# Kernel optimization log

Hardware: AMD Instinct MI355X
Metric: run time of the kernel (lower is better)

## Reference

```python
import jax, jax.numpy as jnp
from jax import lax
import numpy as np

B, NG, NC = 4, 513, 512  # batch, grid size N, coef size N-1

_STENCILS = [[[-1/6, 2/3], [-1/3, -1/6]],
             [[2/3, -1/6], [-1/6, -1/3]],
             [[-1/6, -1/3], [2/3, -1/6]],
             [[-1/3, -1/6], [-1/6, 2/3]]]

def _kernel():
    # torch: vstack 4 (1,1,2,2) kernels -> permute(1,0,2,3) => (out=1, in=4, 2, 2)
    return jnp.asarray(_STENCILS, jnp.float32)[None]

def darcy(x, a, kernel):
    # x: (B,1,N,N), a: (B,1,N-1,N-1)
    N = x.shape[-1]
    X = jnp.concatenate([x[:, :, 1:N, :N-1] * a,
                         x[:, :, 1:N, 1:] * a,
                         x[:, :, :N-1, 1:] * a,
                         x[:, :, :N-1, :N-1] * a], axis=1)  # (B,4,N-1,N-1)
    Ax = lax.conv_general_dilated(X, kernel, (1, 1), 'VALID')  # (B,1,N-2,N-2)
    return jnp.pad(Ax, ((0, 0), (0, 0), (1, 1), (1, 1)))

def _conv3(x, w):
    # x: (Cin,H,W), w: (Cout,Cin,3,3), padding=1
    return lax.conv_general_dilated(x[None], w, (1, 1), ((1, 1), (1, 1)))[0]
_CONVB = jax.vmap(_conv3)

def mcc(x, w):
    # per-sample complex 3x3 conv == torch multi_channel_conv diagonal trick
    yr = _CONVB(x.real, w.real) - _CONVB(x.imag, w.imag)
    yi = _CONVB(x.real, w.imag) + _CONVB(x.imag, w.real)
    return yr + 1j * yi

def conjT(w):
    # transpose(-4,-3).transpose(-2,-1).conj()
    return jnp.conj(jnp.swapaxes(jnp.swapaxes(w, 1, 2), -2, -1))

def expand(r):
    Bb, C, M, N = r.shape
    Z = jnp.zeros((Bb, C, 2 * (M + 1), 2 * (N + 1)), r.dtype)
    Z = Z.at[:, :, 1:M+1, 1:N+1].set(r)
    Z = Z.at[:, :, M+2:, 1:N+1].set(-r[:, :, ::-1, :])
    Z = Z.at[:, :, 1:M+1, N+2:].set(-r[:, :, :, ::-1])
    Z = Z.at[:, :, M+2:, N+2:].set(r[:, :, ::-1, ::-1])
    kg = jnp.arange(-M - 1, N + 1, dtype=jnp.float32) * jnp.float32(np.pi)
    ik2 = 1.0 / (kg[:, None] ** 2 + kg[None, :] ** 2)
    ik2 = ik2.at[M + 1, N + 1].set(1.0)
    N2 = 2 * (N + 1)
    lo = N2 // 2 - N2 // 4
    hi = N2 // 2 + N2 // 4 + 1
    return Z, ik2[lo:hi, lo:hi][None, None]

def H_apply(r, w1, w2, w3, wt):
    N1 = r.shape[-1]
    rsym, ik2 = expand(r)
    N2 = rsym.shape[-1]
    lo = N2 // 2 - N2 // 4
    hi = N2 // 2 + N2 // 4 + 1
    rh = jnp.fft.fftshift(jnp.fft.ifft2(rsym, axes=(2, 3)), axes=(2, 3))[:, :, lo:hi, lo:hi]
    for w in (w1, w2, w3):
        rh = mcc(rh, w)
    out = rh * wt * ik2
    for w in (conjT(w3), conjT(w2), conjT(w1)):
        out = mcc(out, w)
    pl = N2 // 4 + 1
    pr = N2 - N2 // 2 - pl
    out = jnp.pad(out, ((0, 0), (0, 0), (pl, pr), (pl, pr)))
    e = jnp.fft.fft2(jnp.fft.ifftshift(out, axes=(2, 3)), axes=(2, 3)).real
    return e[:, :, :N1, :N1]

def fns_step(x, f, a, dinv, kernel, ws):
    # Jacobi smoother, w=3/4, M=10
    for _ in range(10):
        r = f - darcy(x, a, kernel)
        x = x.at[:, :, 1:-1, 1:-1].add(0.75 * dinv * r[:, :, 1:-1, 1:-1])
    r = f - darcy(x, a, kernel)
    e = H_apply(r[:, :, 1:-1, 1:-1], *ws)
    e = jnp.pad(e, ((0, 0), (0, 0), (1, 1), (1, 1)))
    Ae = darcy(e, a, kernel)
    alpha = (jnp.sum(r * e, axis=(1, 2, 3)) / jnp.sum(Ae * e, axis=(1, 2, 3)))[:, None, None, None]
    return x + alpha * e

def _forward(f, coef, w1, w2, w3, wt, K):
    kernel = _kernel()
    diag_k = (2.0 / 3.0) * jnp.ones((1, 1, 2, 2), jnp.float32)
    dinv = 1.0 / lax.conv_general_dilated(coef, diag_k, (1, 1), 'VALID')
    ws = (w1, w2, w3, wt)
    x = jnp.zeros_like(f)
    for _ in range(K):
        x = fns_step(x, f, coef, dinv, kernel, ws)
    r = f - darcy(x, coef, kernel)
    return jnp.linalg.norm(r.reshape(-1)) / jnp.linalg.norm(f.reshape(-1))

def setup_inputs():
    key = jax.random.key(0)
    ks = jax.random.split(key, 12)
    s = jnp.float32(0.1)
    inp = {
        'f': jax.random.normal(ks[0], (B, 1, NG, NG), jnp.float32),
        'coef': jax.random.uniform(ks[1], (B, 1, NC, NC), jnp.float32) + 0.1,
        'u': jnp.zeros((B, 1, NG, NG), jnp.float32),
        'w1r': jax.random.normal(ks[2], (B, 4, 1, 3, 3), jnp.float32) * s,
        'w1i': jax.random.normal(ks[3], (B, 4, 1, 3, 3), jnp.float32) * s,
        'w2r': jax.random.normal(ks[4], (B, 4, 4, 3, 3), jnp.float32) * s,
        'w2i': jax.random.normal(ks[5], (B, 4, 4, 3, 3), jnp.float32) * s,
        'w3r': jax.random.normal(ks[6], (B, 1, 4, 3, 3), jnp.float32) * s,
        'w3i': jax.random.normal(ks[7], (B, 1, 4, 3, 3), jnp.float32) * s,
        'wtr': jax.random.normal(ks[8], (B, 1, NG, NG), jnp.float32) * s,
        'wti': jax.random.normal(ks[9], (B, 1, NG, NG), jnp.float32) * s,
        'epoch': 101,
    }
    return inp

def reference(f, coef, u, w1r, w1i, w2r, w2i, w3r, w3i, wtr, wti, epoch):
    K = (epoch - 1) // 100 + 1
    w1 = w1r + 1j * w1i
    w2 = w2r + 1j * w2i
    w3 = w3r + 1j * w3i
    wt = wtr + 1j * wti
    return _forward(f, coef, w1, w2, w3, wt, K)
```

## Files before the change

### kernel.cpp

```cpp
#include <hip/hip_runtime.h>
#include <math.h>

#ifndef M_PI
#define M_PI 3.14159265358979323846
#endif

#define NGRID 513
#define NCELL 512
#define NINT  511
#define NB    4

constexpr int N2G = NGRID * NGRID;
constexpr int NI2 = NINT * NINT;
constexpr int NQ  = 257 * 257;

#define LDSW 42

typedef unsigned short ushort;
typedef unsigned int uint32;
typedef __attribute__((ext_vector_type(8))) short short8;
typedef __attribute__((ext_vector_type(8))) unsigned short ushort8;
typedef __attribute__((ext_vector_type(4))) float f32x4;

__device__ __forceinline__ ushort f2bf(float x) {
    unsigned u = __float_as_uint(x);
    unsigned r = u + 0x7FFFu + ((u >> 16) & 1u);
    return (ushort)(r >> 16);
}
__device__ __forceinline__ float bf2f(ushort h) {
    return __uint_as_float(((unsigned)h) << 16);
}

__device__ __forceinline__ float rhq_read(const float* __restrict__ rq,
                                          int i, int j) {
    float s = 1.0f;
    if (i > 256) { i = 512 - i; s = -s; }
    if (j > 256) { j = 512 - j; s = -s; }
    return s * rq[i * 257 + j];
}

__device__ __forceinline__ float2 scale_wt(float x0, float x1, float wr, float wi,
                                           int gr, int gc) {
    int du = gr - 256, dv = gc - 256;
    float ik2;
    if (du == 0 && dv == 0)
        ik2 = 1.0f;
    else
        ik2 = (float)(1.0 / (9.869604401089358 * (double)(du * du + dv * dv)));
    return make_float2((x0 * wr - x1 * wi) * ik2, (x0 * wi + x1 * wr) * ik2);
}

__device__ __forceinline__ float darcyA(const float* __restrict__ x,
                                        const float* __restrict__ a,
                                        int i, int j) {
    const float c23 = 2.0f / 3.0f, c16 = 1.0f / 6.0f, c13 = 1.0f / 3.0f;
    float a00 = a[(i - 1) * NCELL + (j - 1)];
    float a01 = a[(i - 1) * NCELL + j];
    float a10 = a[i * NCELL + (j - 1)];
    float a11 = a[i * NCELL + j];
    const float* xm = x + (i - 1) * NGRID;
    const float* xc = x + i * NGRID;
    const float* xp = x + (i + 1) * NGRID;
    return c23 * (a00 + a01 + a10 + a11) * xc[j]
         - c16 * ((a00 + a01) * xm[j] + (a10 + a11) * xp[j]
                + (a00 + a10) * xc[j - 1] + (a01 + a11) * xc[j + 1])
         - c13 * (a00 * xm[j - 1] + a01 * xm[j + 1]
                + a10 * xp[j - 1] + a11 * xp[j + 1]);
}

template <int RES>
__global__ __launch_bounds__(256) void k_jacobi5R(
    const float* __restrict__ xin, const float* __restrict__ a,
    const float* __restrict__ f, const float* __restrict__ dinv,
    float* __restrict__ out, float* __restrict__ rout,
    ushort* __restrict__ tBh, ushort* __restrict__ tBl) {
    constexpr int H  = RES ? 6 : 5;
    constexpr int SX = 16 + 2 * H;
    constexpr int SA = SX - 1;
    constexpr int SF = 16 + 2 * (H - 1);
    __shared__ float sx[SX][SX];
    __shared__ float sa[SA][SA + 1];
    __shared__ float sf[SF][SF];
    __shared__ float sd[SF][SF];
    __shared__ float sp[2][SF][SF + 2];
    __shared__ float st[16][17];
    const float c23 = 2.0f / 3.0f, c16 = 1.0f / 6.0f, c13 = 1.0f / 3.0f;
    int b = blockIdx.z;
    const float* xb = xin + (long long)b * N2G;
    const float* ab = a + (long long)b * NCELL * NCELL;
    const float* fb = f + (long long)b * N2G;
    const float* db = dinv + (long long)b * NI2;
    int ox = blockIdx.x * 16, oy = blockIdx.y * 16;
    int tx = threadIdx.x, ty = threadIdx.y;
    int tid = ty * 16 + tx;

    for (int idx = tid; idx < SX * SX; idx += 256) {
        int ly = idx / SX, lx = idx % SX;
        int gy = oy - H + ly, gx = ox - H + lx;
        bool in = (gy >= 0 && gy < NGRID && gx >= 0 && gx < NGRID);
        sx[ly][lx] = in ? xb[(long long)gy * NGRID + gx] : 0.0f;
    }
    for (int idx = tid; idx < SA * SA; idx += 256) {
        int ly = idx / SA, lx = idx % SA;
        int gy = oy - H + ly, gx = ox - H + lx;
        bool in = (gy >= 0 && gy < NCELL && gx >= 0 && gx < NCELL);
        sa[ly][lx] = in ? ab[(long long)gy * NCELL + gx] : 0.0f;
    }
    for (int idx = tid; idx < SF * SF; idx += 256) {
        int ly = idx / SF, lx = idx % SF;
        int gy = oy - (H - 1) + ly, gx = ox - (H - 1) + lx;
        bool ing = (gy >= 0 && gy < NGRID && gx >= 0 && gx < NGRID);
        bool itr = (gy >= 1 && gy <= NINT && gx >= 1 && gx <= NINT);
        sf[ly][lx] = ing ? fb[(long long)gy * NGRID + gx] : 0.0f;
        sd[ly][lx] = itr ? db[(long long)(gy - 1) * NINT + (gx - 1)] : 0.0f;
    }
    __syncthreads();

    for (int idx = tid; idx < SF * SF; idx += 256) {
        int ly = idx / SF, lx = idx % SF;
        int gy = oy - (H - 1) + ly, gx = ox - (H - 1) + lx;
        float v = 0.0f;
        if (gy >= 0 && gy < NGRID && gx >= 0 && gx < NGRID) {
            float xc = sx[ly + 1][lx + 1];
            if (gy >= 1 && gy <= NINT && gx >= 1 && gx <= NINT) {
                float a00 = sa[ly][lx], a01 = sa[ly][lx + 1];
                float a10 = sa[ly + 1][lx], a11 = sa[ly + 1][lx + 1];
                float Ax = c23 * (a00 + a01 + a10 + a11) * xc
                    - c16 * ((a00 + a01) * sx[ly][lx + 1] + (a10 + a11) * sx[ly + 2][lx + 1]
                           + (a00 + a10) * sx[ly + 1][lx] + (a01 + a11) * sx[ly + 1][lx + 2])
                    - c13 * (a00 * sx[ly][lx] + a01 * sx[ly][lx + 2]
                           + a10 * sx[ly + 2][lx] + a11 * sx[ly + 2][lx + 2]);
                v = xc + 0.75f * sd[ly][lx] * (sf[ly][lx] - Ax);
            } else {
                v = xc;
            }
        }
        sp[0][ly][lx] = v;
    }
    __syncthreads();

    #pragma unroll 1
    for (int s = 2; s <= 5; ++s) {
        int sz = 16 + 2 * (H - s);
        int cur = (s - 1) & 1, prv = s & 1;
        for (int idx = tid; idx < sz * sz; idx += 256) {
            int ly = idx / sz, lx = idx % sz;
            int gy = oy - (H - s) + ly, gx = ox - (H - s) + lx;
            float v = 0.0f;
            if (gy >= 0 && gy < NGRID && gx >= 0 && gx < NGRID) {
                float xc = sp[prv][ly + 1][lx + 1];
                if (gy >= 1 && gy <= NINT && gx >= 1 && gx <= NINT) {
                    int ar = ly + s - 1, ac = lx + s - 1;
                    float a00 = sa[ar][ac], a01 = sa[ar][ac + 1];
                    float a10 = sa[ar + 1][ac], a11 = sa[ar + 1][ac + 1];
                    float Ax = c23 * (a00 + a01 + a10 + a11) * xc
                        - c16 * ((a00 + a01) * sp[prv][ly][lx + 1] + (a10 + a11) * sp[prv][ly + 2][lx + 1]
                               + (a00 + a10) * sp[prv][ly + 1][lx] + (a01 + a11) * sp[prv][ly + 1][lx + 2])
                        - c13 * (a00 * sp[prv][ly][lx] + a01 * sp[prv][ly][lx + 2]
                               + a10 * sp[prv][ly + 2][lx] + a11 * sp[prv][ly + 2][lx + 2]);
                    int fr = ly + s - 1, fc = lx + s - 1;
                    v = xc + 0.75f * sd[fr][fc] * (sf[fr][fc] - Ax);
                } else {
                    v = xc;
                }
            }
            sp[cur][ly][lx] = v;
        }
        __syncthreads();
    }

    int gy = oy + ty, gx = ox + tx;
    long long gidx = (long long)b * N2G + (long long)gy * NGRID + gx;
    if constexpr (!RES) {
        if (gy < NGRID && gx < NGRID) out[gidx] = sp[0][ty][tx];
    } else {
        float rv = 0.0f;
        if (gy < NGRID && gx < NGRID) {
            float x5 = sp[0][ty + 1][tx + 1];
            out[gidx] = x5;
            if (gy >= 1 && gy <= NINT && gx >= 1 && gx <= NINT) {
                float a00 = sa[ty + 5][tx + 5], a01 = sa[ty + 5][tx + 6];
                float a10 = sa[ty + 6][tx + 5], a11 = sa[ty + 6][tx + 6];
                float Ax = c23 * (a00 + a01 + a10 + a11) * x5
                    - c16 * ((a00 + a01) * sp[0][ty][tx + 1] + (a10 + a11) * sp[0][ty + 2][tx + 1]
                           + (a00 + a10) * sp[0][ty + 1][tx] + (a01 + a11) * sp[0][ty + 1][tx + 2])
                    - c13 * (a00 * sp[0][ty][tx] + a01 * sp[0][ty][tx + 2]
                           + a10 * sp[0][ty + 2][tx] + a11 * sp[0][ty + 2][tx + 2]);
                rv = sf[ty + 5][tx + 5] - Ax;
            } else {
                rv = sf[ty + 5][tx + 5];
            }
            rout[gidx] = rv;
        }
        st[ty][tx] = rv;
        __syncthreads();
        int i2 = blockIdx.y * 16 + tx;
        int j2 = blockIdx.x * 16 + ty;
        if (i2 >= 1 && i2 <= NINT && j2 >= 1 && j2 <= NINT) {
            float r2 = st[tx][ty];
            ushort h = f2bf(r2);
            long long o = (long long)b * 511 * 512
                        + (long long)(j2 - 1) * 512 + (i2 - 1);
            tBh[o] = h;
            tBl[o] = f2bf(r2 - bf2f(h));
        }
    }
}

__global__ void k_tables(double* __restrict__ tabD, double* __restrict__ tabC,
                         double* __restrict__ tabS) {
    int t = blockIdx.x * 256 + threadIdx.x;
    if (t < 1024) tabD[t] = sin((M_PI / 512.0) * (double)t);
    if (t < 1025) {
        double ang = (2.0 * M_PI / 1025.0) * (double)t;
        tabC[t] = cos(ang);
        tabS[t] = sin(ang);
    }
}

__device__ __forceinline__ void wsplit(double v, ushort* Dh, ushort* Dl,
                                       long long idx) {
    float vf = (float)v;
    ushort h = f2bf(vf);
    Dh[idx] = h;
    Dl[idx] = f2bf(vf - bf2f(h));
}

constexpr long long R_DSTA = 513LL * 512;
constexpr long long R_DSTB = 513LL * 512;
constexpr long long R_FA   = 511LL * 1056;
constexpr long long R_FB   = 1022LL * 1056;
constexpr long long R_DINV = (long long)NB * NI2;
constexpr long long R_TOT  = R_DSTA + R_DSTB + R_FA + R_FB + R_DINV;

__global__ void k_genAll(const double* __restrict__ tabD,
                         const double* __restrict__ tabC,
                         const double* __restrict__ tabS,
                         const float* __restrict__ coef,
                         float* __restrict__ dinv,
                         ushort* __restrict__ GAh, ushort* __restrict__ GAl,
                         ushort* __restrict__ GBh, ushort* __restrict__ GBl,
                         ushort* __restrict__ FAh, ushort* __restrict__ FAl,
                         ushort* __restrict__ FBh, ushort* __restrict__ FBl) {
    long long gid = (long long)blockIdx.x * 256 + threadIdx.x;
    if (gid < R_DSTA) {
        int idx = (int)gid;
        int u = idx / 512, k = idx % 512;
        double v = 0.0;
        if (k < 511) {
            int t = ((u - 256) * (k + 1)) % 1024;
            if (t < 0) t += 1024;
            v = tabD[t];
        }
        wsplit(v, GAh, GAl, idx);
        return;
    }
    gid -= R_DSTA;
    if (gid < R_DSTB) {
        int idx = (int)gid;
        int v2 = idx / 512, k = idx % 512;
        double val = 0.0;
        if (k < 511) {
            int t = ((v2 - 256) * (k + 1)) % 1024;
            if (t < 0) t += 1024;
            val = tabD[t] * (-1.0 / 262144.0);
        }
        wsplit(val, GBh, GBl, idx);
        return;
    }
    gid -= R_DSTB;
    if (gid < R_FA) {
        int idx = (int)gid;
        int y = idx / 1056, k = idx % 1056;
        double v = 0.0;
        if (k < 1026) {
            int m = (k < 513) ? k : (k - 513);
            long t = ((long)y * (m - 255)) % 1025;
            if (t < 0) t += 1025;
            v = (k < 513) ? tabC[t] : -tabS[t];
        }
        wsplit(v, FAh, FAl, idx);
        return;
    }
    gid -= R_FA;
    if (gid < R_FB) {
        int idx = (int)gid;
        int n = idx / 1056, k = idx % 1056;
        double v = 0.0;
        if (k < 1026) {
            int m = (k < 513) ? k : (k - 513);
            int y = (n < 511) ? n : (n - 511);
            long t = ((long)y * (m - 255)) % 1025;
            if (t < 0) t += 1025;
            bool ktop = (k < 513), nleft = (n < 511);
            if (ktop && nleft)        v = tabC[t];
            else if (ktop && !nleft)  v = -tabS[t];
            else if (!ktop && nleft)  v = tabS[t];
            else                      v = tabC[t];
        }
        wsplit(v, FBh, FBl, idx);
        return;
    }
    gid -= R_FB;
    if (gid < R_DINV) {
        long long idx = gid;
        int b = (int)(idx / NI2);
        int rem = (int)(idx % NI2);
        int p = rem / NINT, q = rem % NINT;
        const float* ab = coef + (long long)b * NCELL * NCELL;
        float s = ab[p * NCELL + q] + ab[p * NCELL + q + 1]
                + ab[(p + 1) * NCELL + q] + ab[(p + 1) * NCELL + q + 1];
        dinv[idx] = 1.0f / ((2.0f / 3.0f) * s);
    }
}

__global__ void k_redA(const float* __restrict__ P, int nsplit, int Mr,
                       ushort* __restrict__ Dh, ushort* __restrict__ Dl) {
    int b = blockIdx.y;
    int idx = blockIdx.x * 256 + threadIdx.x;
    if (idx >= Mr * 512) return;
    int m = idx / 512, k = idx % 512;
    float v = 0.0f;
    if (k < 511) {
        long long base = (long long)m * 511 + k;
        long long str = (long long)Mr * 511;
        #pragma unroll 4
        for (int s = 0; s < nsplit; ++s)
            v += P[((long long)b * nsplit + s) * str + base];
    }
    long long o = (long long)b * Mr * 512 + idx;
    ushort h = f2bf(v);
    Dh[o] = h;
    Dl[o] = f2bf(v - bf2f(h));
}

__global__ void k_redBt(const float* __restrict__ P, int nsplit,
                        ushort* __restrict__ Dh, ushort* __restrict__ Dl) {
    int b = blockIdx.y;
    int idx = blockIdx.x * 256 + threadIdx.x;
    if (idx >= 511 * 1056) return;
    int n = idx / 1056, k = idx % 1056;
    float v = 0.0f;
    if (k < 1026) {
        int row = (k < 513) ? n : (511 + n);
        int col = (k < 513) ? k : (k - 513);
        long long base = (long long)row * 513 + col;
        float acc = 0.0f;
        #pragma unroll 4
        for (int s = 0; s < nsplit; ++s)
            acc += P[((long long)b * nsplit + s) * (1022LL * 513) + base];
        v = (k < 513) ? acc : -acc;
    }
    long long o = (long long)b * 511 * 1056 + idx;
    ushort h = f2bf(v);
    Dh[o] = h;
    Dl[o] = f2bf(v - bf2f(h));
}

__global__ __launch_bounds__(256) void k_mgemm(
    const ushort* __restrict__ Ah, const ushort* __restrict__ Al, long long bsA,
    const ushort* __restrict__ Bh, const ushort* __restrict__ Bl, long long bsB,
    float* __restrict__ C, long long bsC,
    int M, int N, int Kp, int nsplit) {
    __shared__ ushort sAh[128 * LDSW];
    __shared__ ushort sAl[128 * LDSW];
    __shared__ ushort sBh[128 * LDSW];
    __shared__ ushort sBl[128 * LDSW];

    int bz = blockIdx.z, b = bz / nsplit, ks = bz % nsplit;
    int kchunk = (((Kp + nsplit - 1) / nsplit) + 31) & ~31;
    int kbeg = ks * kchunk;
    int kend = min(Kp, kbeg + kchunk);

    Ah += b * bsA; Al += b * bsA;
    Bh += b * bsB; Bl += b * bsB;
    C += ((long long)b * nsplit + ks) * bsC;

    int bm = blockIdx.y * 128, bn = blockIdx.x * 128;
    int tid = threadIdx.x;
    int wave = tid >> 6, lane = tid & 63;
    int wm = (wave >> 1) * 64, wn = (wave & 1) * 64;
    int quad = lane >> 4, l16 = lane & 15;

    f32x4 zf = {0.f, 0.f, 0.f, 0.f};
    f32x4 acc[4][4];
    #pragma unroll
    for (int i = 0; i < 4; ++i)
        #pragma unroll
        for (int j = 0; j < 4; ++j) acc[i][j] = zf;

    int srow = tid >> 2;
    int sk8 = (tid & 3) * 8;

    for (int kt = kbeg; kt < kend; kt += 32) {
        #pragma unroll
        for (int h = 0; h < 2; ++h) {
            int row = srow + 64 * h;
            ushort8 vh = {0, 0, 0, 0, 0, 0, 0, 0};
            ushort8 vl = {0, 0, 0, 0, 0, 0, 0, 0};
            int gm = bm + row;
            if (gm < M) {
                vh = *(const ushort8*)(Ah + (long long)gm * Kp + kt + sk8);
                vl = *(const ushort8*)(Al + (long long)gm * Kp + kt + sk8);
            }
            *(ushort8*)(sAh + row * LDSW + sk8) = vh;
            *(ushort8*)(sAl + row * LDSW + sk8) = vl;
            ushort8 wh = {0, 0, 0, 0, 0, 0, 0, 0};
            ushort8 wl = {0, 0, 0, 0, 0, 0, 0, 0};
            int gn = bn + row;
            if (gn < N) {
                wh = *(const ushort8*)(Bh + (long long)gn * Kp + kt + sk8);
                wl = *(const ushort8*)(Bl + (long long)gn * Kp + kt + sk8);
            }
            *(ushort8*)(sBh + row * LDSW + sk8) = wh;
            *(ushort8*)(sBl + row * LDSW + sk8) = wl;
        }
        __syncthreads();

        short8 afh[4], afl[4], bfh[4], bfl[4];
        #pragma unroll
        for (int t = 0; t < 4; ++t) {
            int ar = wm + t * 16 + l16;
            afh[t] = *(const short8*)(sAh + ar * LDSW + quad * 8);
            afl[t] = *(const short8*)(sAl + ar * LDSW + quad * 8);
            int br = wn + t * 16 + l16;
            bfh[t] = *(const short8*)(sBh + br * LDSW + quad * 8);
            bfl[t] = *(const short8*)(sBl + br * LDSW + quad * 8);
        }
        #pragma unroll
        for (int mt = 0; mt < 4; ++mt)
            #pragma unroll
            for (int nt = 0; nt < 4; ++nt) {
                acc[mt][nt] = __builtin_amdgcn_mfma_f32_16x16x32_bf16(
                    afh[mt], bfh[nt], acc[mt][nt], 0, 0, 0);
                acc[mt][nt] = __builtin_amdgcn_mfma_f32_16x16x32_bf16(
                    afh[mt], bfl[nt], acc[mt][nt], 0, 0, 0);
                acc[mt][nt] = __builtin_amdgcn_mfma_f32_16x16x32_bf16(
                    afl[mt], bfh[nt], acc[mt][nt], 0, 0, 0);
            }
        __syncthreads();
    }

    #pragma unroll
    for (int mt = 0; mt < 4; ++mt) {
        #pragma unroll
        for (int r = 0; r < 4; ++r) {
            int gm = bm + wm + mt * 16 + quad * 4 + r;
            if (gm >= M) continue;
            long long rowoff = (long long)gm * N;
            #pragma unroll
            for (int nt = 0; nt < 4; ++nt) {
                int gn = bn + wn + nt * 16 + l16;
                if (gn < N) C[rowoff + gn] = acc[mt][nt][r];
            }
        }
    }
}

__global__ void k_reduce(const float* __restrict__ Pr,
                         float* __restrict__ outR,
                         int MN, int N, int ldo, long long bsOut, int nsplit) {
    int b = blockIdx.y;
    for (int idx = blockIdx.x * 256 + threadIdx.x; idx < MN;
         idx += gridDim.x * 256) {
        float sr = 0.0f;
        #pragma unroll 4
        for (int s = 0; s < nsplit; ++s)
            sr += Pr[((long long)b * nsplit + s) * MN + idx];
        int m = idx / N, n = idx - m * N;
        outR[(long long)b * bsOut + (long long)m * ldo + n] = sr;
    }
}

__device__ __forceinline__ float2 cmul(float2 a, float2 b) {
    return make_float2(a.x * b.x - a.y * b.y, a.x * b.y + a.y * b.x);
}

__global__ void k_compose(const float* __restrict__ w1r, const float* __restrict__ w1i,
                          const float* __restrict__ w2r, const float* __restrict__ w2i,
                          const float* __restrict__ w3r, const float* __restrict__ w3i,
                          float* __restrict__ kc) {
    int chain = blockIdx.x, b = blockIdx.y;
    int tid = threadIdx.x;
    __shared__ float2 sW1[4][9], sW2[16][9], sW3[4][9], sW21[4][25];
    for (int idx = tid; idx < 36; idx += 128) {
        int c = idx / 9, s = idx % 9, p = s / 3, q = s % 3;
        if (chain == 0) {
            int i1 = b * 36 + c * 9 + p * 3 + q;
            sW1[c][s] = make_float2(w1r[i1], w1i[i1]);
            sW3[c][s] = make_float2(w3r[i1], w3i[i1]);
        } else {
            int it = b * 36 + c * 9 + q * 3 + p;
            sW1[c][s] = make_float2(w3r[it], -w3i[it]);
            sW3[c][s] = make_float2(w1r[it], -w1i[it]);
        }
    }
    for (int idx = tid; idx < 144; idx += 128) {
        int co = idx / 36, r = idx % 36, ci = r / 9, s = r % 9, p = s / 3, q = s % 3;
        int iw = (chain == 0) ? (b * 144 + co * 36 + ci * 9 + p * 3 + q)
                              : (b * 144 + ci * 36 + co * 9 + q * 3 + p);
        float iv = w2i[iw];
        sW2[co * 4 + ci][s] = make_float2(w2r[iw], (chain == 0) ? iv : -iv);
    }
    __syncthreads();
    for (int idx = tid; idx < 100; idx += 128) {
        int cm = idx / 25, r = idx % 25, di = r / 5 - 2, dj = r % 5 - 2;
        float2 acc = make_float2(0.f, 0.f);
        for (int c1 = 0; c1 < 4; ++c1)
            for (int p = 0; p < 3; ++p)
                for (int q = 0; q < 3; ++q) {
                    int ei = di - (p - 1) + 1, ej = dj - (q - 1) + 1;
                    if (ei >= 0 && ei < 3 && ej >= 0 && ej < 3) {
                        float2 t = cmul(sW2[cm * 4 + c1][p * 3 + q], sW1[c1][ei * 3 + ej]);
                        acc.x += t.x; acc.y += t.y;
                    }
                }
        sW21[cm][r] = acc;
    }
    __syncthreads();
    for (int idx = tid; idx < 49; idx += 128) {
        int di = idx / 7 - 3, dj = idx % 7 - 3;
        float2 acc = make_float2(0.f, 0.f);
        for (int cm = 0; cm < 4; ++cm)
            for (int p = 0; p < 3; ++p)
                for (int q = 0; q < 3; ++q) {
                    int ei = di - (p - 1), ej = dj - (q - 1);
                    if (ei >= -2 && ei <= 2 && ej >= -2 && ej <= 2) {
                        float2 t = cmul(sW3[cm][p * 3 + q], sW21[cm][(ei + 2) * 5 + (ej + 2)]);
                        acc.x += t.x; acc.y += t.y;
                    }
                }
        ((float2*)kc)[(b * 2 + chain) * 49 + idx] = acc;
    }
}

template <int MODE>
__global__ __launch_bounds__(256) void k_conv7(
    const float* __restrict__ xr, const float* __restrict__ xi,
    const float* __restrict__ wtr, const float* __restrict__ wti,
    const float* __restrict__ kc,
    float* __restrict__ outr, float* __restrict__ outi,
    ushort* __restrict__ oAh, ushort* __restrict__ oAl) {
    constexpr bool CPLX = (MODE == 1);
    __shared__ float2 tile[38][23];
    __shared__ float2 kt[49];
    int b = blockIdx.z;
    int tid = threadIdx.y * 16 + threadIdx.x;
    const float2* kb = (const float2*)kc + (b * 2 + MODE) * 49;
    for (int idx = tid; idx < 49; idx += 256) kt[idx] = kb[idx];
    int row_base = blockIdx.y * 32 - 3;
    int col_base = blockIdx.x * 16 - 3;
    const float* rq = xr + (long long)b * NQ;
    for (int idx = tid; idx < 38 * 22; idx += 256) {
        int r = idx / 22, c = idx % 22;
        int gr = row_base + r, gc = col_base + c;
        float vr = 0.0f, vi = 0.0f;
        if (gr >= 0 && gr < NGRID && gc >= 0 && gc < NGRID) {
            if (MODE == 0) {
                vr = rhq_read(rq, gr, gc);
            } else {
                long long g = (long long)b * N2G + (long long)gr * NGRID + gc;
                float2 sc = scale_wt(xr[g], xi[g], wtr[g], wti[g], gr, gc);
                vr = sc.x; vi = sc.y;
            }
        }
        tile[r][c] = make_float2(vr, vi);
    }
    __syncthreads();

    int tx = threadIdx.x, r0 = threadIdx.y * 2;
    float2 acc[2];
    acc[0] = make_float2(0.f, 0.f);
    acc[1] = make_float2(0.f, 0.f);
    #pragma unroll
    for (int t = 0; t < 7; ++t) {
        float2 kv[7];
        #pragma unroll
        for (int s = 0; s < 7; ++s) kv[s] = kt[s * 7 + t];
        #pragma unroll
        for (int rr = 0; rr < 8; ++rr) {
            float2 xv = tile[r0 + rr][tx + t];
            #pragma unroll
            for (int s = 0; s < 7; ++s) {
                int orow = rr - s;
                if (orow >= 0 && orow < 2) {
                    acc[orow].x += kv[s].x * xv.x;
                    acc[orow].y += kv[s].y * xv.x;
                    if (CPLX) {
                        acc[orow].x -= kv[s].y * xv.y;
                        acc[orow].y += kv[s].x * xv.y;
                    }
                }
            }
        }
    }
    int gc = blockIdx.x * 16 + tx;
    if (gc >= NGRID) return;
    #pragma unroll
    for (int r = 0; r < 2; ++r) {
        int gr = blockIdx.y * 32 + r0 + r;
        if (gr < NGRID) {
            if (MODE == 0) {
                long long g = (long long)b * N2G + (long long)gr * NGRID + gc;
                outr[g] = acc[r].x;
                outi[g] = acc[r].y;
            } else {
                long long o = (long long)b * 513 * 1056
                            + (long long)gr * 1056 + gc;
                ushort h = f2bf(acc[r].x);
                oAh[o] = h;
                oAl[o] = f2bf(acc[r].x - bf2f(h));
                ushort h2 = f2bf(acc[r].y);
                oAh[o + 513] = h2;
                oAl[o + 513] = f2bf(acc[r].y - bf2f(h2));
            }
        }
    }
}

template <int CHAIN>
__global__ __launch_bounds__(256) void k_ring7(
    const float* __restrict__ xr, const float* __restrict__ xi,
    const float* __restrict__ wtr, const float* __restrict__ wti,
    const float* __restrict__ w1r, const float* __restrict__ w1i,
    const float* __restrict__ w2r, const float* __restrict__ w2i,
    const float* __restrict__ w3r, const float* __restrict__ w3i,
    float* __restrict__ outr, float* __restrict__ outi,
    ushort* __restrict__ oAh, ushort* __restrict__ oAl) {
    constexpr bool CPLX = (CHAIN == 1);
    __shared__ float2 W1s[4][9], W2s[16][9], W3s[4][9];
    __shared__ float2 Y[4][4][68];
    __shared__ float2 Z[4][3][66];
    int side = blockIdx.y, b = blockIdx.z;
    int u0 = blockIdx.x * 64;
    int ulo = (side < 2) ? 0 : 2;
    int uhi = (side < 2) ? (NGRID - 1) : (NGRID - 3);
    if (u0 > uhi) return;
    int tid = threadIdx.x;
    const float* rq = xr + (long long)b * NQ;

    for (int idx = tid; idx < 36; idx += 256) {
        int c = idx / 9, s = idx % 9, p = s / 3, q = s % 3;
        if (CHAIN == 0) {
            int i1 = b * 36 + c * 9 + p * 3 + q;
            W1s[c][s] = make_float2(w1r[i1], w1i[i1]);
            W3s[c][s] = make_float2(w3r[i1], w3i[i1]);
        } else {
            int it = b * 36 + c * 9 + q * 3 + p;
            W1s[c][s] = make_float2(w3r[it], -w3i[it]);
            W3s[c][s] = make_float2(w1r[it], -w1i[it]);
        }
    }
    for (int idx = tid; idx < 144; idx += 256) {
        int co = idx / 36, r = idx % 36, ci = r / 9, s = r % 9, p = s / 3, q = s % 3;
        int iw = (CHAIN == 0) ? (b * 144 + co * 36 + ci * 9 + p * 3 + q)
                              : (b * 144 + ci * 36 + co * 9 + q * 3 + p);
        float iv = w2i[iw];
        W2s[co * 4 + ci][s] = make_float2(w2r[iw], (CHAIN == 0) ? iv : -iv);
    }
    __syncthreads();

    for (int idx = tid; idx < 4 * 4 * 68; idx += 256) {
        int ch = idx / (4 * 68), r = idx % (4 * 68), d = r / 68, uu = r % 68;
        int u = u0 - 2 + uu;
        float2 acc = make_float2(0.f, 0.f);
        if (u >= 0 && u < NGRID) {
            int i, j;
            if (side == 0)      { i = d;       j = u; }
            else if (side == 1) { i = 512 - d; j = u; }
            else if (side == 2) { i = u;       j = d; }
            else                { i = u;       j = 512 - d; }
            for (int p = 0; p < 3; ++p)
                for (int q = 0; q < 3; ++q) {
                    int ii = i + p - 1, jj = j + q - 1;
                    if (ii >= 0 && ii < NGRID && jj >= 0 && jj < NGRID) {
                        float vr, vi;
                        if (CHAIN == 0) {
                            vr = rhq_read(rq, ii, jj);
                            vi = 0.0f;
                        } else {
                            long long g = (long long)b * N2G
                                        + (long long)ii * NGRID + jj;
                            float2 sc = scale_wt(xr[g], xi[g], wtr[g], wti[g],
                                                 ii, jj);
                            vr = sc.x; vi = sc.y;
                        }
                        float2 w = W1s[ch][p * 3 + q];
                        acc.x += w.x * vr - w.y * vi;
                        acc.y += w.x * vi + w.y * vr;
                    }
                }
        }
        Y[ch][d][uu] = acc;
    }
    __syncthreads();

    for (int idx = tid; idx < 4 * 3 * 66; idx += 256) {
        int co = idx / (3 * 66), r = idx % (3 * 66), d = r / 66, uu = r % 66;
        int u = u0 - 1 + uu;
        float2 acc = make_float2(0.f, 0.f);
        if (u >= 0 && u < NGRID) {
            for (int p = 0; p < 3; ++p)
                for (int q = 0; q < 3; ++q) {
                    int dd, du;
                    if (side == 0)      { dd = p - 1; du = q - 1; }
                    else if (side == 1) { dd = 1 - p; du = q - 1; }
                    else if (side == 2) { dd = q - 1; du = p - 1; }
                    else                { dd = 1 - q; du = p - 1; }
                    int d2 = d + dd, uy = uu + 1 + du;
                    if (d2 >= 0) {
                        for (int ci = 0; ci < 4; ++ci) {
                            float2 yv = Y[ci][d2][uy];
                            float2 w = W2s[co * 4 + ci][p * 3 + q];
                            acc.x += w.x * yv.x - w.y * yv.y;
                            acc.y += w.x * yv.y + w.y * yv.x;
                        }
                    }
                }
        }
        Z[co][d][uu] = acc;
    }
    __syncthreads();

    for (int idx = tid; idx < 128; idx += 256) {
        int d = idx / 64, uu = idx % 64;
        int u = u0 + uu;
        if (u < ulo || u > uhi) continue;
        float2 acc = make_float2(0.f, 0.f);
        for (int p = 0; p < 3; ++p)
            for (int q = 0; q < 3; ++q) {
                int dd, du;
                if (side == 0)      { dd = p - 1; du = q - 1; }
                else if (side == 1) { dd = 1 - p; du = q - 1; }
                else if (side == 2) { dd = q - 1; du = p - 1; }
                else                { dd = 1 - q; du = p - 1; }
                int d2 = d + dd, uz = uu + 1 + du;
                if (d2 >= 0) {
                    for (int ci = 0; ci < 4; ++ci) {
                        float2 zv = Z[ci][d2][uz];
                        float2 w = W3s[ci][p * 3 + q];
                        acc.x += w.x * zv.x - w.y * zv.y;
                        acc.y += w.x * zv.y + w.y * zv.x;
                    }
                }
            }
        int i, j;
        if (side == 0)      { i = d;       j = u; }
        else if (side == 1) { i = 512 - d; j = u; }
        else if (side == 2) { i = u;       j = d; }
        else                { i = u;       j = 512 - d; }
        if (CHAIN == 0) {
            long long g = (long long)b * N2G + (long long)i * NGRID + j;
            outr[g] = acc.x;
            outi[g] = acc.y;
        } else {
            long long o = (long long)b * 513 * 1056 + (long long)i * 1056 + j;
            ushort h = f2bf(acc.x);
            oAh[o] = h;
            oAl[o] = f2bf(acc.x - bf2f(h));
            ushort h2 = f2bf(acc.y);
            oAh[o + 513] = h2;
            oAl[o + 513] = f2bf(acc.y - bf2f(h2));
        }
    }
}

__global__ void k_dotAe(const float* __restrict__ r, const float* __restrict__ e,
                        const float* __restrict__ a, float* __restrict__ red) {
    int b = blockIdx.y;
    const float* rb = r + (long long)b * N2G;
    const float* eb = e + (long long)b * N2G;
    const float* ab = a + (long long)b * NCELL * NCELL;
    float s1 = 0.0f, s2 = 0.0f;
    for (int idx = blockIdx.x * blockDim.x + threadIdx.x; idx < NI2;
         idx += gridDim.x * blockDim.x) {
        int i = idx / NINT + 1, j = idx % NINT + 1;
        long long g = (long long)i * NGRID + j;
        float ev = eb[g];
        float Ax = darcyA(eb, ab, i, j);
        s1 += rb[g] * ev;
        s2 += Ax * ev;
    }
    #pragma unroll
    for (int o = 32; o > 0; o >>= 1) {
        s1 += __shfl_down(s1, o);
        s2 += __shfl_down(s2, o);
    }
    __shared__ float l1[4], l2[4];
    int wid = threadIdx.x >> 6;
    if ((threadIdx.x & 63) == 0) { l1[wid] = s1; l2[wid] = s2; }
    __syncthreads();
    if (threadIdx.x == 0) {
        atomicAdd(&red[2 * b], l1[0] + l1[1] + l1[2] + l1[3]);
        atomicAdd(&red[2 * b + 1], l2[0] + l2[1] + l2[2] + l2[3]);
    }
}

__global__ void k_update(float* __restrict__ x, const float* __restrict__ e,
                         const float* __restrict__ red) {
    long long idx = (long long)blockIdx.x * blockDim.x + threadIdx.x;
    if (idx >= (long long)NB * N2G) return;
    int b = (int)(idx / N2G);
    float alpha = red[2 * b] / red[2 * b + 1];
    x[idx] += alpha * e[idx];
}

__global__ void k_fin(const float* __restrict__ x, const float* __restrict__ e,
                      const float* __restrict__ f, const float* __restrict__ a,
                      float* __restrict__ red) {
    const float c23 = 2.0f / 3.0f, c16 = 1.0f / 6.0f, c13 = 1.0f / 3.0f;
    int b = blockIdx.y;
    long long base = (long long)b * N2G;
    const float* ab = a + (long long)b * NCELL * NCELL;
    float alpha = red[8 + 2 * b] / red[8 + 2 * b + 1];
    float s1 = 0.0f, s2 = 0.0f;
    for (int idx = blockIdx.x * blockDim.x + threadIdx.x; idx < N2G;
         idx += gridDim.x * blockDim.x) {
        int i = idx / NGRID, j = idx - i * NGRID;
        float fv = f[base + idx];
        float rv = fv;
        if (i >= 1 && i <= NINT && j >= 1 && j <= NINT) {
            float a00 = ab[(i - 1) * NCELL + (j - 1)];
            float a01 = ab[(i - 1) * NCELL + j];
            float a10 = ab[i * NCELL + (j - 1)];
            float a11 = ab[i * NCELL + j];
            long long gm = base + (long long)(i - 1) * NGRID + j;
            long long gc = base + (long long)i * NGRID + j;
            long long gp = base + (long long)(i + 1) * NGRID + j;
            float xmm = x[gm - 1] + alpha * e[gm - 1];
            float xm0 = x[gm] + alpha * e[gm];
            float xmp = x[gm + 1] + alpha * e[gm + 1];
            float xcm = x[gc - 1] + alpha * e[gc - 1];
            float xc0 = x[gc] + alpha * e[gc];
            float xcp = x[gc + 1] + alpha * e[gc + 1];
            float xpm = x[gp - 1] + alpha * e[gp - 1];
            float xp0 = x[gp] + alpha * e[gp];
            float xpp = x[gp + 1] + alpha * e[gp + 1];
            float Ax = c23 * (a00 + a01 + a10 + a11) * xc0
                - c16 * ((a00 + a01) * xm0 + (a10 + a11) * xp0
                       + (a00 + a10) * xcm + (a01 + a11) * xcp)
                - c13 * (a00 * xmm + a01 * xmp + a10 * xpm + a11 * xpp);
            rv = fv - Ax;
        }
        s1 += rv * rv;
        s2 += fv * fv;
    }
    #pragma unroll
    for (int o = 32; o > 0; o >>= 1) {
        s1 += __shfl_down(s1, o);
        s2 += __shfl_down(s2, o);
    }
    __shared__ float l1[4], l2[4];
    int wid = threadIdx.x >> 6;
    if ((threadIdx.x & 63) == 0) { l1[wid] = s1; l2[wid] = s2; }
    __syncthreads();
    if (threadIdx.x == 0) {
        atomicAdd(&red[16], l1[0] + l1[1] + l1[2] + l1[3]);
        atomicAdd(&red[17], l2[0] + l2[1] + l2[2] + l2[3]);
    }
}

__global__ void k_final(const float* __restrict__ red, float* __restrict__ out) {
    out[0] = sqrtf(red[16] / red[17]);
}

extern "C" void kernel_launch(void* const* d_in, const int* in_sizes, int n_in,
                              void* d_out, int out_size, void* d_ws, size_t ws_size,
                              hipStream_t stream) {
    (void)in_sizes; (void)n_in; (void)out_size; (void)ws_size;
    const float* f    = (const float*)d_in[0];
    const float* coef = (const float*)d_in[1];
    const float* w1r  = (const float*)d_in[3];
    const float* w1i  = (const float*)d_in[4];
    const float* w2r  = (const float*)d_in[5];
    const float* w2i  = (const float*)d_in[6];
    const float* w3r  = (const float*)d_in[7];
    const float* w3i  = (const float*)d_in[8];
    const float* wtr  = (const float*)d_in[9];
    const float* wti  = (const float*)d_in[10];
    float* out = (float*)d_out;

    float* ws = (float*)d_ws;
    size_t off = 0;
    auto alloc = [&](long long n) {
        float* p = ws + off;
        off += (size_t)((n + 3) & ~3LL);
        return p;
    };
    float* x0   = alloc((long long)NB * N2G);
    float* x1   = alloc((long long)NB * N2G);
    float* rr   = alloc((long long)NB * N2G);
    float* ee   = alloc((long long)NB * N2G);
    float* dinv = alloc((long long)NB * NI2);
    float* c1r  = alloc((long long)NB * 4 * N2G);
    float* c1i  = alloc((long long)NB * 4 * N2G);
    float* c2r  = alloc((long long)NB * 4 * N2G);
    float* c2i  = alloc((long long)NB * 4 * N2G);
    float* pr   = c1r;
    float* or_  = alloc((long long)NB * N2G);
    float* oi_  = alloc((long long)NB * N2G);
    float* rhq  = alloc((long long)NB * NQ);
    float* red  = alloc(20);
    ushort* sGh  = (ushort*)alloc(513 * 512 / 2);
    ushort* sGl  = (ushort*)alloc(513 * 512 / 2);
    ushort* sGth = (ushort*)alloc(513 * 512 / 2);
    ushort* sGtl = (ushort*)alloc(513 * 512 / 2);
    ushort* sFAh = (ushort*)alloc(511 * 1056 / 2);
    ushort* sFAl = (ushort*)alloc(511 * 1056 / 2);
    ushort* sFBh = (ushort*)alloc(1022 * 1056 / 2);
    ushort* sFBl = (ushort*)alloc(1022 * 1056 / 2);
    ushort* dA2h = (ushort*)alloc((long long)NB * 257 * 512 / 2);
    ushort* dA2l = (ushort*)alloc((long long)NB * 257 * 512 / 2);
    ushort* dA3h = (ushort*)alloc((long long)NB * 513 * 1056 / 2);
    ushort* dA3l = (ushort*)alloc((long long)NB * 513 * 1056 / 2);
    ushort* dB1h = (ushort*)alloc((long long)NB * 511 * 512 / 2);
    ushort* dB1l = (ushort*)alloc((long long)NB * 511 * 512 / 2);
    ushort* dB4h = (ushort*)alloc((long long)NB * 511 * 1056 / 2);
    ushort* dB4l = (ushort*)alloc((long long)NB * 511 * 1056 / 2);
    float* kcomp = alloc(NB * 2 * 49 * 2);
    double* tabD = (double*)alloc(1024 * 2);
    double* tabC = (double*)alloc(1026 * 2);
    double* tabS = (double*)alloc(1026 * 2);

    dim3 blk2(16, 16);
    dim3 grdS(33, 33, NB);
    dim3 grdC(33, 17, NB);
    dim3 grdR(9, 4, NB);
    const int SP = 4;

    hipMemsetAsync(x0, 0, (size_t)NB * N2G * sizeof(float), stream);
    hipMemsetAsync(ee, 0, (size_t)NB * N2G * sizeof(float), stream);
    hipMemsetAsync(red, 0, 20 * sizeof(float), stream);
    hipMemsetAsync(dA3h, 0, (size_t)NB * 513 * 1056 * 2 * 2, stream);
    hipMemsetAsync(dB1h, 0, (size_t)NB * 511 * 512 * 2 * 2, stream);
    k_tables<<<dim3(5), dim3(256), 0, stream>>>(tabD, tabC, tabS);
    k_genAll<<<dim3((unsigned)((R_TOT + 255) / 256)), dim3(256), 0, stream>>>(
        tabD, tabC, tabS, coef, dinv,
        sGh, sGl, sGth, sGtl, sFAh, sFAl, sFBh, sFBl);
    k_compose<<<dim3(2, NB), dim3(128), 0, stream>>>(w1r, w1i, w2r, w2i, w3r, w3i, kcomp);

    for (int step = 0; step < 2; ++step) {
        k_jacobi5R<0><<<grdS, blk2, 0, stream>>>(
            x0, coef, f, dinv, x1, nullptr, nullptr, nullptr);
        k_jacobi5R<1><<<grdS, blk2, 0, stream>>>(
            x1, coef, f, dinv, x0, rr, dB1h, dB1l);

        k_mgemm<<<dim3(4, 3, NB * SP), dim3(256), 0, stream>>>(
            sGh, sGl, 0, dB1h, dB1l, (long long)511 * 512,
            pr, (long long)257 * 511, 257, 511, 512, SP);
        k_redA<<<dim3((257 * 512 + 255) / 256, NB), dim3(256), 0, stream>>>(
            pr, SP, 257, dA2h, dA2l);
        k_mgemm<<<dim3(3, 3, NB * SP), dim3(256), 0, stream>>>(
            dA2h, dA2l, (long long)257 * 512, sGth, sGtl, 0,
            pr, (long long)NQ, 257, 257, 512, SP);
        k_reduce<<<dim3(259, NB), dim3(256), 0, stream>>>(
            pr, rhq, NQ, 257, 257, (long long)NQ, SP);

        k_conv7<0><<<grdC, blk2, 0, stream>>>(
            rhq, nullptr, nullptr, nullptr, kcomp, or_, oi_, nullptr, nullptr);
        k_ring7<0><<<grdR, dim3(256), 0, stream>>>(
            rhq, nullptr, nullptr, nullptr,
            w1r, w1i, w2r, w2i, w3r, w3i, or_, oi_, nullptr, nullptr);
        k_conv7<1><<<grdC, blk2, 0, stream>>>(
            or_, oi_, wtr, wti, kcomp, nullptr, nullptr, dA3h, dA3l);
        k_ring7<1><<<grdR, dim3(256), 0, stream>>>(
            or_, oi_, wtr, wti,
            w1r, w1i, w2r, w2i, w3r, w3i, nullptr, nullptr, dA3h, dA3l);

        k_mgemm<<<dim3(5, 8, NB * 4), dim3(256), 0, stream>>>(
            sFBh, sFBl, 0, dA3h, dA3l, (long long)513 * 1056,
            pr, 1022LL * 513, 1022, 513, 1056, 4);
        k_redBt<<<dim3(2109, NB), dim3(256), 0, stream>>>(pr, 4, dB4h, dB4l);
        k_mgemm<<<dim3(4, 4, NB * SP), dim3(256), 0, stream>>>(
            sFAh, sFAl, 0, dB4h, dB4l, (long long)511 * 1056,
            pr, (long long)NI2, 511, 511, 1056, SP);
        k_reduce<<<dim3(1024, NB), dim3(256), 0, stream>>>(
            pr, ee + NGRID + 1, NI2, NINT, NGRID, (long long)N2G, SP);

        k_dotAe<<<dim3(128, NB), dim3(256), 0, stream>>>(
            rr, ee, coef, red + 8 * step);
        if (step == 0)
            k_update<<<dim3((NB * N2G + 255) / 256), dim3(256), 0, stream>>>(
                x0, ee, red);
    }
    k_fin<<<dim3(128, NB), dim3(256), 0, stream>>>(x0, ee, f, coef, red);
    k_final<<<dim3(1), dim3(1), 0, stream>>>(red, out);
}
```

Measured before the change: 690.6 us.

## Prefetch next GEMM K-tile into registers while MFMAs run

```diff
diff --git a/kernel.cpp b/kernel.cpp
--- a/kernel.cpp
+++ b/kernel.cpp
@@ -14,7 +14,7 @@
 constexpr int NI2 = NINT * NINT;
 constexpr int NQ  = 257 * 257;
 
-#define LDSW 42
+#define LDSW 40
 
 typedef unsigned short ushort;
 typedef unsigned int uint32;
@@ -391,31 +391,48 @@
 
     int srow = tid >> 2;
     int sk8 = (tid & 3) * 8;
+    bool inA0 = (bm + srow) < M,       inB0 = (bn + srow) < N;
+    bool inA1 = (bm + srow + 64) < M,  inB1 = (bn + srow + 64) < N;
+    const ushort* gA0h = Ah + (long long)(bm + srow) * Kp + sk8;
+    const ushort* gA0l = Al + (long long)(bm + srow) * Kp + sk8;
+    const ushort* gA1h = gA0h + 64LL * Kp;
+    const ushort* gA1l = gA0l + 64LL * Kp;
+    const ushort* gB0h = Bh + (long long)(bn + srow) * Kp + sk8;
+    const ushort* gB0l = Bl + (long long)(bn + srow) * Kp + sk8;
+    const ushort* gB1h = gB0h + 64LL * Kp;
+    const ushort* gB1l = gB0l + 64LL * Kp;
+
+    ushort8 z8 = {0, 0, 0, 0, 0, 0, 0, 0};
+    ushort8 pAh0, pAl0, pAh1, pAl1, pBh0, pBl0, pBh1, pBl1;
+
+    auto load_tile = [&](int kt) {
+        pAh0 = inA0 ? *(const ushort8*)(gA0h + kt) : z8;
+        pAl0 = inA0 ? *(const ushort8*)(gA0l + kt) : z8;
+        pAh1 = inA1 ? *(const ushort8*)(gA1h + kt) : z8;
+        pAl1 = inA1 ? *(const ushort8*)(gA1l + kt) : z8;
+        pBh0 = inB0 ? *(const ushort8*)(gB0h + kt) : z8;
+        pBl0 = inB0 ? *(const ushort8*)(gB0l + kt) : z8;
+        pBh1 = inB1 ? *(const ushort8*)(gB1h + kt) : z8;
+        pBl1 = inB1 ? *(const ushort8*)(gB1l + kt) : z8;
+    };
+    auto store_tile = [&]() {
+        *(ushort8*)(sAh + srow * LDSW + sk8) = pAh0;
+        *(ushort8*)(sAl + srow * LDSW + sk8) = pAl0;
+        *(ushort8*)(sAh + (srow + 64) * LDSW + sk8) = pAh1;
+        *(ushort8*)(sAl + (srow + 64) * LDSW + sk8) = pAl1;
+        *(ushort8*)(sBh + srow * LDSW + sk8) = pBh0;
+        *(ushort8*)(sBl + srow * LDSW + sk8) = pBl0;
+        *(ushort8*)(sBh + (srow + 64) * LDSW + sk8) = pBh1;
+        *(ushort8*)(sBl + (srow + 64) * LDSW + sk8) = pBl1;
+    };
+
+    load_tile(kbeg);
+    store_tile();
+    __syncthreads();
 
     for (int kt = kbeg; kt < kend; kt += 32) {
-        #pragma unroll
-        for (int h = 0; h < 2; ++h) {
-            int row = srow + 64 * h;
-            ushort8 vh = {0, 0, 0, 0, 0, 0, 0, 0};
-            ushort8 vl = {0, 0, 0, 0, 0, 0, 0, 0};
-            int gm = bm + row;
-            if (gm < M) {
-                vh = *(const ushort8*)(Ah + (long long)gm * Kp + kt + sk8);
-                vl = *(const ushort8*)(Al + (long long)gm * Kp + kt + sk8);
-            }
-            *(ushort8*)(sAh + row * LDSW + sk8) = vh;
-            *(ushort8*)(sAl + row * LDSW + sk8) = vl;
-            ushort8 wh = {0, 0, 0, 0, 0, 0, 0, 0};
-            ushort8 wl = {0, 0, 0, 0, 0, 0, 0, 0};
-            int gn = bn + row;
-            if (gn < N) {
-                wh = *(const ushort8*)(Bh + (long long)gn * Kp + kt + sk8);
-                wl = *(const ushort8*)(Bl + (long long)gn * Kp + kt + sk8);
-            }
-            *(ushort8*)(sBh + row * LDSW + sk8) = wh;
-            *(ushort8*)(sBl + row * LDSW + sk8) = wl;
-        }
-        __syncthreads();
+        bool more = (kt + 32) < kend;
+        if (more) load_tile(kt + 32);
 
         short8 afh[4], afl[4], bfh[4], bfl[4];
         #pragma unroll
@@ -438,6 +455,8 @@
                 acc[mt][nt] = __builtin_amdgcn_mfma_f32_16x16x32_bf16(
                     afl[mt], bfh[nt], acc[mt][nt], 0, 0, 0);
             }
+        __syncthreads();
+        if (more) store_tile();
         __syncthreads();
     }
 
```

After: 660.4 us. 4.4% less time.
